# Performance work log

Measured on AMD Instinct MI355X. Metric: run time of the kernel, lower is better.

## Reference

```python
import jax, jax.numpy as jnp
from jax import lax
import numpy as np

B, L1, L2, H = 32, 128, 512, 256


def setup_inputs() -> dict:
    key = jax.random.key(0)
    ks = jax.random.split(key, 20)
    # valid lengths guarantee every row has at least one unmasked y position
    xlen = jax.random.randint(ks[0], (B,), L1 // 2, L1 + 1)
    ylen = jax.random.randint(ks[1], (B,), L2 // 2, L2 + 1)
    x_mask = (jnp.arange(L1)[None, :] >= xlen[:, None]).astype(jnp.int32)
    y_mask = (jnp.arange(L2)[None, :] >= ylen[:, None]).astype(jnp.int32)
    s = 0.05
    return {
        "x": jax.random.normal(ks[2], (B, L1, H), jnp.float32),
        "x_mask": x_mask,
        "y": jax.random.normal(ks[3], (B, L2, H), jnp.float32),
        "y_mask": y_mask,
        "h0": jax.random.uniform(ks[4], (B, H), jnp.float32),
        "c0": jax.random.uniform(ks[5], (B, H), jnp.float32),
        "Wq": jax.random.normal(ks[6], (H, H), jnp.float32) * s,
        "bq": jax.random.normal(ks[7], (H,), jnp.float32) * s,
        "Wup": jax.random.normal(ks[8], (H, H), jnp.float32) * s,
        "bup": jax.random.normal(ks[9], (H,), jnp.float32) * s,
        "Wvp": jax.random.normal(ks[10], (H, H), jnp.float32) * s,
        "bvp": jax.random.normal(ks[11], (H,), jnp.float32) * s,
        "Vw": jax.random.normal(ks[12], (1, H), jnp.float32) * s,
        "Vb": jax.random.normal(ks[13], (1,), jnp.float32) * s,
        "Wg": jax.random.normal(ks[14], (2 * H, 2 * H), jnp.float32) * s,
        "bg": jax.random.normal(ks[15], (2 * H,), jnp.float32) * s,
        "Wih": jax.random.normal(ks[16], (4 * H, 2 * H), jnp.float32) * s,
        "Whh": jax.random.normal(ks[17], (4 * H, H), jnp.float32) * s,
        "bih": jax.random.normal(ks[18], (4 * H,), jnp.float32) * s,
        "bhh": jax.random.normal(ks[19], (4 * H,), jnp.float32) * s,
    }


def _match_rnn(x, xm, y, ym, h0, c0, Wq, bq, Wup, bup, Wvp, bvp, Vw, Vb,
               Wg, bg, Wih, Whh, bih, bhh):
    # hoist time-invariant projections (original recomputes W_q(y) every step)
    y_proj = jnp.einsum("bld,hd->blh", y, Wq) + bq        # [B,L2,H]
    x_up = jnp.einsum("btd,hd->bth", x, Wup) + bup        # [B,L1,H]
    v = Vw[0]

    def step(carry, inp):
        h, c = carry
        x_t, xup_t, xm_t = inp                            # [B,H],[B,H],[B]
        hid = jnp.dot(h, Wvp.T) + bvp                     # [B,H]
        e = jnp.tanh(xup_t[:, None, :] + y_proj + hid[:, None, :])  # [B,L2,H]
        s = jnp.einsum("blh,h->bl", e, v) + Vb[0]         # [B,L2]
        s = jnp.where(ym, -jnp.inf, s)
        alpha = jax.nn.softmax(s, axis=-1)
        ct = jnp.einsum("bl,bld->bd", alpha, y)           # [B,H]
        merge = jnp.concatenate([x_t, ct], axis=-1)       # [B,2H]
        gt = jax.nn.sigmoid(jnp.dot(merge, Wg.T) + bg)
        li = jnp.where(xm_t[:, None], 0.0, gt * merge)
        # torch.nn.LSTMCell gate order: i, f, g, o
        gates = jnp.dot(li, Wih.T) + bih + jnp.dot(h, Whh.T) + bhh
        i, f, g, o = jnp.split(gates, 4, axis=-1)
        c_new = jax.nn.sigmoid(f) * c + jax.nn.sigmoid(i) * jnp.tanh(g)
        h_new = jax.nn.sigmoid(o) * jnp.tanh(c_new)
        h_new = jnp.where(xm_t[:, None], 0.0, h_new)
        return (h_new, c_new), h_new

    xs = (jnp.swapaxes(x, 0, 1), jnp.swapaxes(x_up, 0, 1),
          jnp.swapaxes(xm, 0, 1))
    _, hs = lax.scan(step, (h0, c0), xs)                  # hs: [L1,B,H]
    return jnp.swapaxes(hs, 0, 1)                         # [B,L1,H]


def reference(x, x_mask, y, y_mask, h0, c0, Wq, bq, Wup, bup, Wvp, bvp,
              Vw, Vb, Wg, bg, Wih, Whh, bih, bhh):
    xm = x_mask.astype(bool)
    ym = y_mask.astype(bool)
    return _match_rnn(x, xm, y, ym, h0, c0, Wq, bq, Wup, bup, Wvp, bvp,
                      Vw, Vb, Wg, bg, Wih, Whh, bih, bhh)
```

## Files before the change

### kernel.cpp

```cpp
#include <hip/hip_runtime.h>
#include <hip/hip_bf16.h>


#define B_ 32
#define L1_ 128
#define L2_ 512
#define H_ 256
#define GRP 8
#define TB 512
#define LOG2E_ 1.4426950408889634f

#define YP_OFF   0u
#define XUP_OFF  (8u << 20)
#define QP_OFF   (10u << 20)
#define CTP_OFF  (QP_OFF + (256u << 10))
#define ES_OFF   (CTP_OFF + (256u << 10))
#define LI_OFF   (ES_OFF + (4u << 10))
#define HB_OFF   (LI_OFF + (64u << 10))
#define BAR_OFF  (HB_OFF + (32u << 10))
#define WGB_OFF  (BAR_OFF + (4u << 10))
#define WIHB_OFF (WGB_OFF + (512u << 10))
#define WHHB_OFF (WIHB_OFF + (1024u << 10))

__device__ __forceinline__ float fexp2(float x) {
#if __has_builtin(__builtin_amdgcn_exp2f)
  return __builtin_amdgcn_exp2f(x);
#else
  return exp2f(x);
#endif
}
__device__ __forceinline__ float frcp(float x) {
#if __has_builtin(__builtin_amdgcn_rcpf)
  return __builtin_amdgcn_rcpf(x);
#else
  return 1.0f / x;
#endif
}
__device__ __forceinline__ float ftanh(float x) {
  return 1.0f - 2.0f * frcp(1.0f + fexp2(x * (2.0f * LOG2E_)));
}
__device__ __forceinline__ float fsig(float x) {
  return frcp(1.0f + fexp2(-x * LOG2E_));
}
__device__ __forceinline__ float dot4(float4 a, float4 b) {
  return a.x * b.x + a.y * b.y + a.z * b.z + a.w * b.w;
}
__device__ __forceinline__ float bfl(unsigned u) {
  return __uint_as_float(u << 16);
}
__device__ __forceinline__ float bfh(unsigned u) {
  return __uint_as_float(u & 0xffff0000u);
}
__device__ __forceinline__ unsigned short f2bf(float f) {
  __hip_bfloat16 b = __float2bfloat16(f);
  return *reinterpret_cast<unsigned short*>(&b);
}

__device__ __forceinline__ float cload(const float* p) {
  return __hip_atomic_load(p, __ATOMIC_RELAXED, __HIP_MEMORY_SCOPE_AGENT);
}
__device__ __forceinline__ void cstore(float* p, float v) {
  __hip_atomic_store(p, v, __ATOMIC_RELAXED, __HIP_MEMORY_SCOPE_AGENT);
}

__device__ __forceinline__ void group_barrier(unsigned* cnt, unsigned target) {
  asm volatile("s_waitcnt vmcnt(0)" ::: "memory");
  __syncthreads();
  if (threadIdx.x == 0) {
    __hip_atomic_fetch_add(cnt, 1u, __ATOMIC_RELAXED,
                           __HIP_MEMORY_SCOPE_AGENT);
    while (__hip_atomic_load(cnt, __ATOMIC_RELAXED,
                             __HIP_MEMORY_SCOPE_AGENT) < GRP * target) {
      __builtin_amdgcn_s_sleep(1);
    }
  }
  __syncthreads();
  asm volatile("" ::: "memory");
}

__global__ __launch_bounds__(256) void proj_kernel(
    const float* __restrict__ y, const float* __restrict__ Wq,
    const float* __restrict__ bq, const float* __restrict__ x,
    const float* __restrict__ Wup, const float* __restrict__ bup,
    __hip_bfloat16* __restrict__ yp, __hip_bfloat16* __restrict__ xup) {
  __shared__ float As[32 * 256];
  const int blk = blockIdx.x;
  const int tid = threadIdx.x;
  const float* src;
  const float* W;
  const float* bias;
  __hip_bfloat16* dst;
  int row0;
  if (blk < 512) {
    src = y; W = Wq; bias = bq; dst = yp; row0 = blk * 32;
  } else {
    src = x; W = Wup; bias = bup; dst = xup; row0 = (blk - 512) * 32;
  }
  const float4* s4 = (const float4*)(src + (size_t)row0 * H_);
  float4* A4 = (float4*)As;
#pragma unroll
  for (int i = 0; i < 8; ++i) A4[i * 256 + tid] = s4[i * 256 + tid];
  __syncthreads();

  const float4* w4 = (const float4*)(W + (size_t)tid * H_);
  float acc[32];
#pragma unroll
  for (int r = 0; r < 32; ++r) acc[r] = 0.0f;
  for (int kc = 0; kc < 64; ++kc) {
    float4 w = w4[kc];
#pragma unroll
    for (int r = 0; r < 32; ++r) acc[r] += dot4(A4[r * 64 + kc], w);
  }
  const float bb = bias[tid];
#pragma unroll 4
  for (int r = 0; r < 32; ++r)
    dst[(size_t)(row0 + r) * H_ + tid] = __float2bfloat16(acc[r] + bb);
}

__global__ __launch_bounds__(256) void wconv_kernel(
    const float* __restrict__ Wg, const float* __restrict__ Wih,
    const float* __restrict__ Whh, unsigned short* __restrict__ wgb,
    unsigned short* __restrict__ wihb, unsigned short* __restrict__ whhb) {
  const int e = blockIdx.x * 256 + threadIdx.x;
  const float* src;
  unsigned short* dst;
  int off;
  if (e < 65536) {
    src = Wg; dst = wgb; off = e;
  } else if (e < 196608) {
    src = Wih; dst = wihb; off = e - 65536;
  } else {
    src = Whh; dst = whhb; off = e - 196608;
  }
  float4 v = ((const float4*)src)[off];
  ushort4 o;
  o.x = f2bf(v.x); o.y = f2bf(v.y); o.z = f2bf(v.z); o.w = f2bf(v.w);
  ((ushort4*)dst)[off] = o;
}

__global__ __launch_bounds__(TB) void scan_kernel(
    const float* __restrict__ x, const int* __restrict__ x_mask,
    const float* __restrict__ y, const int* __restrict__ y_mask,
    const float* __restrict__ h0, const float* __restrict__ c0,
    const float* __restrict__ Wvp, const float* __restrict__ bvp,
    const float* __restrict__ Vw, const float* __restrict__ Vb,
    const float* __restrict__ bg, const float* __restrict__ bih,
    const float* __restrict__ bhh, char* __restrict__ ws,
    float* __restrict__ out) {
  const int blk = blockIdx.x;
  const int b = blk & 31;
  const int g = blk >> 5;
  const int tid = threadIdx.x;

  const __hip_bfloat16* yp = (const __hip_bfloat16*)(ws + YP_OFF);
  const unsigned short* xupb = (const unsigned short*)(ws + XUP_OFF);
  float* qp = (float*)(ws + QP_OFF);
  float* ctp = (float*)(ws + CTP_OFF);
  float* esb = (float*)(ws + ES_OFF);
  float* lib = (float*)(ws + LI_OFF);
  float* hb = (float*)(ws + HB_OFF);
  unsigned* cnt = (unsigned*)(ws + BAR_OFF) + b * 32;
  const unsigned short* wgb = (const unsigned short*)(ws + WGB_OFF);
  const unsigned short* wihb = (const unsigned short*)(ws + WIHB_OFF);
  const unsigned short* whhb = (const unsigned short*)(ws + WHHB_OFF);

  __shared__ uint4 yp_lds[64 * 32];
  __shared__ float y_lds[64 * 256];
  __shared__ __align__(16) float h_s[H_];
  __shared__ float q_s[H_];
  __shared__ float v_s[H_];
  __shared__ float bvp_s[H_];
  __shared__ float e_s[64];
  __shared__ __align__(16) float mg_s[2 * H_];
  __shared__ __align__(16) float li_s[2 * H_];
  __shared__ float gate_s[128];
  __shared__ float red_s[64 * 9];
  __shared__ float esum_s[8];
  __shared__ __align__(16) float c_s[32];
  __shared__ __align__(16) float hn_s[32];
  __shared__ float bg_s[64];
  __shared__ float bi_s[128];
  __shared__ int ym_s[64];
  __shared__ int xm_s[L1_];

  unsigned target = 0;

  {
    const uint4* src = (const uint4*)(yp + (size_t)(b * L2_ + g * 64) * H_);
    for (int k = tid; k < 64 * 32; k += TB) {
      int r = k >> 5, c = k & 31;
      yp_lds[r * 32 + (c ^ (r & 31))] = src[k];
    }
    const float4* ys = (const float4*)(y + (size_t)(b * L2_ + g * 64) * H_);
    float4* yd = (float4*)y_lds;
    for (int k = tid; k < 64 * 64; k += TB) yd[k] = ys[k];
  }
  if (tid < H_) {
    v_s[tid] = Vw[tid];
    bvp_s[tid] = bvp[tid];
  }
  if (tid < 64) {
    ym_s[tid] = y_mask[b * L2_ + g * 64 + tid];
    bg_s[tid] = bg[g * 64 + tid];
  }
  if (tid < 128) {
    xm_s[tid] = x_mask[b * L1_ + tid];
    const int grow = (tid >> 5) * H_ + g * 32 + (tid & 31);
    bi_s[tid] = bih[grow] + bhh[grow];
  }
  if (tid < 32) {
    float hv = h0[b * H_ + g * 32 + tid];
    c_s[tid] = c0[b * H_ + g * 32 + tid];
    hn_s[tid] = hv;
    cstore(&hb[b * H_ + g * 32 + tid], hv);
  }
  const float vb = Vb[0];
  __syncthreads();
  {
    const int j = tid >> 1, sub = tid & 1;
    const float4* w4 =
        (const float4*)(Wvp + (size_t)j * H_ + g * 32 + sub * 16);
    const float4* hv4 = (const float4*)(hn_s + sub * 16);
    float acc = 0.f;
#pragma unroll
    for (int i = 0; i < 4; ++i) acc += dot4(w4[i], hv4[i]);
    acc += __shfl_xor(acc, 1);
    if (sub == 0) cstore(&qp[(b * 8 + g) * H_ + j], acc);
  }
  group_barrier(cnt, ++target);

  for (int t = 0; t < L1_; ++t) {
    const int xm = xm_s[t];

    {
      const int j = tid & 255, half = tid >> 8;
      float acc = 0.f;
#pragma unroll
      for (int k = 0; k < 4; ++k)
        acc += cload(&qp[(b * 8 + half * 4 + k) * H_ + j]);
      red_s[half * 256 + j] = acc;
      if (tid < H_) h_s[tid] = cload(&hb[b * H_ + tid]);
    }
    __syncthreads();
    if (tid < H_) {
      q_s[tid] = red_s[tid] + red_s[256 + tid] + bvp_s[tid] +
                 bfl(xupb[(size_t)(b * L1_ + t) * H_ + tid]);
    }
    __syncthreads();

    {
      const int l = tid & 63, sub = tid >> 6;
      float acc = 0.f;
#pragma unroll
      for (int i = 0; i < 4; ++i) {
        uint4 u = yp_lds[l * 32 + ((sub * 4 + i) ^ (l & 31))];
        const int h = sub * 32 + i * 8;
        acc += v_s[h + 0] * ftanh(q_s[h + 0] + bfl(u.x));
        acc += v_s[h + 1] * ftanh(q_s[h + 1] + bfh(u.x));
        acc += v_s[h + 2] * ftanh(q_s[h + 2] + bfl(u.y));
        acc += v_s[h + 3] * ftanh(q_s[h + 3] + bfh(u.y));
        acc += v_s[h + 4] * ftanh(q_s[h + 4] + bfl(u.z));
        acc += v_s[h + 5] * ftanh(q_s[h + 5] + bfh(u.z));
        acc += v_s[h + 6] * ftanh(q_s[h + 6] + bfl(u.w));
        acc += v_s[h + 7] * ftanh(q_s[h + 7] + bfh(u.w));
      }
      red_s[l * 9 + sub] = acc;
    }
    __syncthreads();
    if (tid < 64) {
      float s = vb;
#pragma unroll
      for (int k = 0; k < 8; ++k) s += red_s[tid * 9 + k];
      float e = ym_s[tid] ? 0.f : fexp2(s * LOG2E_);
      e_s[tid] = e;
      float ss = e;
#pragma unroll
      for (int off = 32; off >= 1; off >>= 1) ss += __shfl_xor(ss, off);
      if (tid == 0) cstore(&esb[b * 8 + g], ss);
    }
    __syncthreads();

    {
      const int d = tid & 255, part = tid >> 8;
      float acc = 0.f;
#pragma unroll 8
      for (int i = 0; i < 32; ++i)
        acc += e_s[part * 32 + i] * y_lds[(part * 32 + i) * 256 + d];
      __syncthreads();
      red_s[tid] = acc;
    }
    __syncthreads();
    if (tid < H_)
      cstore(&ctp[(b * 8 + g) * H_ + tid], red_s[tid] + red_s[tid + 256]);
    group_barrier(cnt, ++target);

    if (tid < 8) esum_s[tid] = cload(&esb[b * 8 + tid]);
    {
      const int j = tid & 255, half = tid >> 8;
      float acc = 0.f;
#pragma unroll
      for (int k = 0; k < 4; ++k)
        acc += cload(&ctp[(b * 8 + half * 4 + k) * H_ + j]);
      red_s[half * 256 + j] = acc;
      if (tid < H_) mg_s[tid] = x[(size_t)(b * L1_ + t) * H_ + tid];
    }
    __syncthreads();
    if (tid < H_) {
      float tot = esum_s[0] + esum_s[1] + esum_s[2] + esum_s[3] + esum_s[4] +
                  esum_s[5] + esum_s[6] + esum_s[7];
      mg_s[H_ + tid] = (red_s[tid] + red_s[256 + tid]) * frcp(tot);
    }
    __syncthreads();

    {
      const int o = tid >> 3, sub = tid & 7;
      const uint4* wrow = (const uint4*)(wgb + (size_t)(g * 64 + o) * 512);
      const float4* m4 = (const float4*)mg_s;
      float acc = 0.f;
#pragma unroll
      for (int j = 0; j < 8; ++j) {
        uint4 u = wrow[sub + 8 * j];
        float4 ma = m4[(sub + 8 * j) * 2], mb = m4[(sub + 8 * j) * 2 + 1];
        acc += bfl(u.x) * ma.x + bfh(u.x) * ma.y + bfl(u.y) * ma.z +
               bfh(u.y) * ma.w + bfl(u.z) * mb.x + bfh(u.z) * mb.y +
               bfl(u.w) * mb.z + bfh(u.w) * mb.w;
      }
      acc += __shfl_xor(acc, 1);
      acc += __shfl_xor(acc, 2);
      acc += __shfl_xor(acc, 4);
      if (sub == 0) {
        float gt = fsig(acc + bg_s[o]);
        cstore(&lib[b * 512 + g * 64 + o], xm ? 0.f : gt * mg_s[g * 64 + o]);
      }
    }
    group_barrier(cnt, ++target);

    li_s[tid] = cload(&lib[b * 512 + tid]);
    __syncthreads();
    {
      const int r = tid >> 2, sub = tid & 3;
      const int grow = (r >> 5) * H_ + g * 32 + (r & 31);
      const uint4* wi = (const uint4*)(wihb + (size_t)grow * 512);
      const uint4* wh = (const uint4*)(whhb + (size_t)grow * 256);
      const float4* l4 = (const float4*)li_s;
      const float4* h4 = (const float4*)h_s;
      float acc = 0.f;
#pragma unroll
      for (int j = 0; j < 16; ++j) {
        uint4 u = wi[sub + 4 * j];
        float4 a = l4[(sub + 4 * j) * 2], c2 = l4[(sub + 4 * j) * 2 + 1];
        acc += bfl(u.x) * a.x + bfh(u.x) * a.y + bfl(u.y) * a.z +
               bfh(u.y) * a.w + bfl(u.z) * c2.x + bfh(u.z) * c2.y +
               bfl(u.w) * c2.z + bfh(u.w) * c2.w;
      }
#pragma unroll
      for (int j = 0; j < 8; ++j) {
        uint4 u = wh[sub + 4 * j];
        float4 a = h4[(sub + 4 * j) * 2], c2 = h4[(sub + 4 * j) * 2 + 1];
        acc += bfl(u.x) * a.x + bfh(u.x) * a.y + bfl(u.y) * a.z +
               bfh(u.y) * a.w + bfl(u.z) * c2.x + bfh(u.z) * c2.y +
               bfl(u.w) * c2.z + bfh(u.w) * c2.w;
      }
      acc += __shfl_xor(acc, 1);
      acc += __shfl_xor(acc, 2);
      if (sub == 0) gate_s[r] = acc + bi_s[r];
    }
    __syncthreads();
    if (tid < 32) {
      float ii = gate_s[tid], ff = gate_s[32 + tid];
      float gg = gate_s[64 + tid], oo = gate_s[96 + tid];
      float cn = fsig(ff) * c_s[tid] + fsig(ii) * ftanh(gg);
      float hn = xm ? 0.f : fsig(oo) * ftanh(cn);
      c_s[tid] = cn;
      hn_s[tid] = hn;
      cstore(&hb[b * H_ + g * 32 + tid], hn);
      out[(size_t)(b * L1_ + t) * H_ + g * 32 + tid] = hn;
    }
    __syncthreads();

    {
      const int j = tid >> 1, sub = tid & 1;
      const float4* w4 =
          (const float4*)(Wvp + (size_t)j * H_ + g * 32 + sub * 16);
      const float4* hv4 = (const float4*)(hn_s + sub * 16);
      float acc = 0.f;
#pragma unroll
      for (int i = 0; i < 4; ++i) acc += dot4(w4[i], hv4[i]);
      acc += __shfl_xor(acc, 1);
      if (sub == 0) cstore(&qp[(b * 8 + g) * H_ + j], acc);
    }
    group_barrier(cnt, ++target);
  }
}

extern "C" void kernel_launch(void* const* d_in, const int* in_sizes, int n_in,
                              void* d_out, int out_size, void* d_ws,
                              size_t ws_size, hipStream_t stream) {
  const float* x = (const float*)d_in[0];
  const int* x_mask = (const int*)d_in[1];
  const float* y = (const float*)d_in[2];
  const int* y_mask = (const int*)d_in[3];
  const float* h0 = (const float*)d_in[4];
  const float* c0 = (const float*)d_in[5];
  const float* Wq = (const float*)d_in[6];
  const float* bq = (const float*)d_in[7];
  const float* Wup = (const float*)d_in[8];
  const float* bup = (const float*)d_in[9];
  const float* Wvp = (const float*)d_in[10];
  const float* bvp = (const float*)d_in[11];
  const float* Vw = (const float*)d_in[12];
  const float* Vb = (const float*)d_in[13];
  const float* Wg = (const float*)d_in[14];
  const float* bg = (const float*)d_in[15];
  const float* Wih = (const float*)d_in[16];
  const float* Whh = (const float*)d_in[17];
  const float* bih = (const float*)d_in[18];
  const float* bhh = (const float*)d_in[19];

  float* out = (float*)d_out;
  char* ws = (char*)d_ws;

  hipMemsetAsync(ws + BAR_OFF, 0, 4096, stream);
  proj_kernel<<<dim3(640), dim3(256), 0, stream>>>(
      y, Wq, bq, x, Wup, bup, (__hip_bfloat16*)(ws + YP_OFF),
      (__hip_bfloat16*)(ws + XUP_OFF));
  wconv_kernel<<<dim3(1024), dim3(256), 0, stream>>>(
      Wg, Wih, Whh, (unsigned short*)(ws + WGB_OFF),
      (unsigned short*)(ws + WIHB_OFF), (unsigned short*)(ws + WHHB_OFF));
  scan_kernel<<<dim3(B_ * GRP), dim3(TB), 0, stream>>>(
      x, x_mask, y, y_mask, h0, c0, Wvp, bvp, Vw, Vb, bg, bih, bhh, ws, out);
}
```

Baseline: 1.539 ms.

## Cut per-step group barriers by replicating LSTM state and splitting gates by K

Each block in a batch group now keeps the full h and c state and recomputes the Wvp·h query projection locally from a bf16 copy of Wvp, so the per-step qp exchange and its group barrier go away. The LSTM gate matmul is split along the input dimension: each block computes partial sums for all 1024 gate rows from its own 64 li values and 32 h values, then writes them to global memory. After one barrier every block reduces the 8 partials and redundantly runs the cell update. This aims to halve inter-block barriers per timestep, in exchange for redundant Wvp work, more global partial-sum traffic and extra LDS use.

After: 2.424 ms. 1.57x slower.

```diff
diff --git a/kernel.cpp b/kernel.cpp
--- a/kernel.cpp
+++ b/kernel.cpp
@@ -12,15 +12,14 @@
 
 #define YP_OFF   0u
 #define XUP_OFF  (8u << 20)
-#define QP_OFF   (10u << 20)
-#define CTP_OFF  (QP_OFF + (256u << 10))
+#define CTP_OFF  (10u << 20)
 #define ES_OFF   (CTP_OFF + (256u << 10))
-#define LI_OFF   (ES_OFF + (4u << 10))
-#define HB_OFF   (LI_OFF + (64u << 10))
-#define BAR_OFF  (HB_OFF + (32u << 10))
+#define GPW_OFF  (ES_OFF + (4u << 10))
+#define BAR_OFF  (GPW_OFF + (1024u << 10))
 #define WGB_OFF  (BAR_OFF + (4u << 10))
 #define WIHB_OFF (WGB_OFF + (512u << 10))
 #define WHHB_OFF (WIHB_OFF + (1024u << 10))
+#define WVPB_OFF (WHHB_OFF + (512u << 10))
 
 __device__ __forceinline__ float fexp2(float x) {
 #if __has_builtin(__builtin_amdgcn_exp2f)
@@ -119,8 +118,9 @@
 
 __global__ __launch_bounds__(256) void wconv_kernel(
     const float* __restrict__ Wg, const float* __restrict__ Wih,
-    const float* __restrict__ Whh, unsigned short* __restrict__ wgb,
-    unsigned short* __restrict__ wihb, unsigned short* __restrict__ whhb) {
+    const float* __restrict__ Whh, const float* __restrict__ Wvp,
+    unsigned short* __restrict__ wgb, unsigned short* __restrict__ wihb,
+    unsigned short* __restrict__ whhb, unsigned short* __restrict__ wvpb) {
   const int e = blockIdx.x * 256 + threadIdx.x;
   const float* src;
   unsigned short* dst;
@@ -129,8 +129,10 @@
     src = Wg; dst = wgb; off = e;
   } else if (e < 196608) {
     src = Wih; dst = wihb; off = e - 65536;
+  } else if (e < 262144) {
+    src = Whh; dst = whhb; off = e - 196608;
   } else {
-    src = Whh; dst = whhb; off = e - 196608;
+    src = Wvp; dst = wvpb; off = e - 262144;
   }
   float4 v = ((const float4*)src)[off];
   ushort4 o;
@@ -142,11 +144,10 @@
     const float* __restrict__ x, const int* __restrict__ x_mask,
     const float* __restrict__ y, const int* __restrict__ y_mask,
     const float* __restrict__ h0, const float* __restrict__ c0,
-    const float* __restrict__ Wvp, const float* __restrict__ bvp,
-    const float* __restrict__ Vw, const float* __restrict__ Vb,
-    const float* __restrict__ bg, const float* __restrict__ bih,
-    const float* __restrict__ bhh, char* __restrict__ ws,
-    float* __restrict__ out) {
+    const float* __restrict__ bvp, const float* __restrict__ Vw,
+    const float* __restrict__ Vb, const float* __restrict__ bg,
+    const float* __restrict__ bih, const float* __restrict__ bhh,
+    char* __restrict__ ws, float* __restrict__ out) {
   const int blk = blockIdx.x;
   const int b = blk & 31;
   const int g = blk >> 5;
@@ -154,36 +155,32 @@
 
   const __hip_bfloat16* yp = (const __hip_bfloat16*)(ws + YP_OFF);
   const unsigned short* xupb = (const unsigned short*)(ws + XUP_OFF);
-  float* qp = (float*)(ws + QP_OFF);
   float* ctp = (float*)(ws + CTP_OFF);
   float* esb = (float*)(ws + ES_OFF);
-  float* lib = (float*)(ws + LI_OFF);
-  float* hb = (float*)(ws + HB_OFF);
+  float* gpw = (float*)(ws + GPW_OFF);
   unsigned* cnt = (unsigned*)(ws + BAR_OFF) + b * 32;
   const unsigned short* wgb = (const unsigned short*)(ws + WGB_OFF);
   const unsigned short* wihb = (const unsigned short*)(ws + WIHB_OFF);
   const unsigned short* whhb = (const unsigned short*)(ws + WHHB_OFF);
+  const unsigned short* wvpb = (const unsigned short*)(ws + WVPB_OFF);
 
   __shared__ uint4 yp_lds[64 * 32];
   __shared__ float y_lds[64 * 256];
   __shared__ __align__(16) float h_s[H_];
+  __shared__ __align__(16) float c_s[H_];
   __shared__ float q_s[H_];
   __shared__ float v_s[H_];
   __shared__ float bvp_s[H_];
+  __shared__ __align__(16) float mg_s[2 * H_];
+  __shared__ __align__(16) float li_s[64];
+  __shared__ float gate_s[1024];
+  __shared__ float bi_s[1024];
+  __shared__ float red_s[64 * 9];
   __shared__ float e_s[64];
-  __shared__ __align__(16) float mg_s[2 * H_];
-  __shared__ __align__(16) float li_s[2 * H_];
-  __shared__ float gate_s[128];
-  __shared__ float red_s[64 * 9];
   __shared__ float esum_s[8];
-  __shared__ __align__(16) float c_s[32];
-  __shared__ __align__(16) float hn_s[32];
   __shared__ float bg_s[64];
-  __shared__ float bi_s[128];
   __shared__ int ym_s[64];
   __shared__ int xm_s[L1_];
-
-  unsigned target = 0;
 
   {
     const uint4* src = (const uint4*)(yp + (size_t)(b * L2_ + g * 64) * H_);
@@ -198,53 +195,40 @@
   if (tid < H_) {
     v_s[tid] = Vw[tid];
     bvp_s[tid] = bvp[tid];
+    h_s[tid] = h0[b * H_ + tid];
+    c_s[tid] = c0[b * H_ + tid];
   }
   if (tid < 64) {
     ym_s[tid] = y_mask[b * L2_ + g * 64 + tid];
     bg_s[tid] = bg[g * 64 + tid];
   }
-  if (tid < 128) {
-    xm_s[tid] = x_mask[b * L1_ + tid];
-    const int grow = (tid >> 5) * H_ + g * 32 + (tid & 31);
-    bi_s[tid] = bih[grow] + bhh[grow];
-  }
-  if (tid < 32) {
-    float hv = h0[b * H_ + g * 32 + tid];
-    c_s[tid] = c0[b * H_ + g * 32 + tid];
-    hn_s[tid] = hv;
-    cstore(&hb[b * H_ + g * 32 + tid], hv);
-  }
+  if (tid < 128) xm_s[tid] = x_mask[b * L1_ + tid];
+  bi_s[tid] = bih[tid] + bhh[tid];
+  bi_s[tid + 512] = bih[tid + 512] + bhh[tid + 512];
   const float vb = Vb[0];
   __syncthreads();
-  {
-    const int j = tid >> 1, sub = tid & 1;
-    const float4* w4 =
-        (const float4*)(Wvp + (size_t)j * H_ + g * 32 + sub * 16);
-    const float4* hv4 = (const float4*)(hn_s + sub * 16);
-    float acc = 0.f;
-#pragma unroll
-    for (int i = 0; i < 4; ++i) acc += dot4(w4[i], hv4[i]);
-    acc += __shfl_xor(acc, 1);
-    if (sub == 0) cstore(&qp[(b * 8 + g) * H_ + j], acc);
-  }
-  group_barrier(cnt, ++target);
+
+  unsigned target = 0;
 
   for (int t = 0; t < L1_; ++t) {
     const int xm = xm_s[t];
 
     {
-      const int j = tid & 255, half = tid >> 8;
+      const int j = tid >> 1, sub = tid & 1;
+      const uint4* wv = (const uint4*)(wvpb + (size_t)j * H_) + sub * 16;
+      const float4* h4 = (const float4*)h_s + sub * 32;
       float acc = 0.f;
 #pragma unroll
-      for (int k = 0; k < 4; ++k)
-        acc += cload(&qp[(b * 8 + half * 4 + k) * H_ + j]);
-      red_s[half * 256 + j] = acc;
-      if (tid < H_) h_s[tid] = cload(&hb[b * H_ + tid]);
-    }
-    __syncthreads();
-    if (tid < H_) {
-      q_s[tid] = red_s[tid] + red_s[256 + tid] + bvp_s[tid] +
-                 bfl(xupb[(size_t)(b * L1_ + t) * H_ + tid]);
+      for (int k = 0; k < 16; ++k) {
+        uint4 u = wv[k];
+        float4 a = h4[2 * k], c2 = h4[2 * k + 1];
+        acc += bfl(u.x) * a.x + bfh(u.x) * a.y + bfl(u.y) * a.z +
+               bfh(u.y) * a.w + bfl(u.z) * c2.x + bfh(u.z) * c2.y +
+               bfl(u.w) * c2.z + bfh(u.w) * c2.w;
+      }
+      acc += __shfl_xor(acc, 1);
+      if (sub == 0)
+        q_s[j] = acc + bvp_s[j] + bfl(xupb[(size_t)(b * L1_ + t) * H_ + j]);
     }
     __syncthreads();
 
@@ -286,7 +270,6 @@
 #pragma unroll 8
       for (int i = 0; i < 32; ++i)
         acc += e_s[part * 32 + i] * y_lds[(part * 32 + i) * 256 + d];
-      __syncthreads();
       red_s[tid] = acc;
     }
     __syncthreads();
@@ -330,66 +313,62 @@
       acc += __shfl_xor(acc, 4);
       if (sub == 0) {
         float gt = fsig(acc + bg_s[o]);
-        cstore(&lib[b * 512 + g * 64 + o], xm ? 0.f : gt * mg_s[g * 64 + o]);
+        li_s[o] = xm ? 0.f : gt * mg_s[g * 64 + o];
       }
     }
+    __syncthreads();
+
+    {
+      const float4* l4 = (const float4*)li_s;
+      const float4* hb4 = (const float4*)(h_s + g * 32);
+#pragma unroll
+      for (int rr = 0; rr < 2; ++rr) {
+        const int r = tid + rr * 512;
+        const uint4* wi = (const uint4*)wihb + (size_t)r * 64 + g * 8;
+        const uint4* wh = (const uint4*)whhb + (size_t)r * 32 + g * 4;
+        float acc = 0.f;
+#pragma unroll
+        for (int j = 0; j < 8; ++j) {
+          uint4 u = wi[j];
+          float4 a = l4[2 * j], c2 = l4[2 * j + 1];
+          acc += bfl(u.x) * a.x + bfh(u.x) * a.y + bfl(u.y) * a.z +
+                 bfh(u.y) * a.w + bfl(u.z) * c2.x + bfh(u.z) * c2.y +
+                 bfl(u.w) * c2.z + bfh(u.w) * c2.w;
+        }
+#pragma unroll
+        for (int j = 0; j < 4; ++j) {
+          uint4 u = wh[j];
+          float4 a = hb4[2 * j], c2 = hb4[2 * j + 1];
+          acc += bfl(u.x) * a.x + bfh(u.x) * a.y + bfl(u.y) * a.z +
+                 bfh(u.y) * a.w + bfl(u.z) * c2.x + bfh(u.z) * c2.y +
+                 bfl(u.w) * c2.z + bfh(u.w) * c2.w;
+        }
+        cstore(&gpw[(size_t)(b * 8 + g) * 1024 + r], acc);
+      }
+    }
     group_barrier(cnt, ++target);
 
-    li_s[tid] = cload(&lib[b * 512 + tid]);
-    __syncthreads();
-    {
-      const int r = tid >> 2, sub = tid & 3;
-      const int grow = (r >> 5) * H_ + g * 32 + (r & 31);
-      const uint4* wi = (const uint4*)(wihb + (size_t)grow * 512);
-      const uint4* wh = (const uint4*)(whhb + (size_t)grow * 256);
-      const float4* l4 = (const float4*)li_s;
-      const float4* h4 = (const float4*)h_s;
-      float acc = 0.f;
-#pragma unroll
-      for (int j = 0; j < 16; ++j) {
-        uint4 u = wi[sub + 4 * j];
-        float4 a = l4[(sub + 4 * j) * 2], c2 = l4[(sub + 4 * j) * 2 + 1];
-        acc += bfl(u.x) * a.x + bfh(u.x) * a.y + bfl(u.y) * a.z +
-               bfh(u.y) * a.w + bfl(u.z) * c2.x + bfh(u.z) * c2.y +
-               bfl(u.w) * c2.z + bfh(u.w) * c2.w;
-      }
-#pragma unroll
-      for (int j = 0; j < 8; ++j) {
-        uint4 u = wh[sub + 4 * j];
-        float4 a = h4[(sub + 4 * j) * 2], c2 = h4[(sub + 4 * j) * 2 + 1];
-        acc += bfl(u.x) * a.x + bfh(u.x) * a.y + bfl(u.y) * a.z +
-               bfh(u.y) * a.w + bfl(u.z) * c2.x + bfh(u.z) * c2.y +
-               bfl(u.w) * c2.z + bfh(u.w) * c2.w;
-      }
-      acc += __shfl_xor(acc, 1);
-      acc += __shfl_xor(acc, 2);
-      if (sub == 0) gate_s[r] = acc + bi_s[r];
-    }
-    __syncthreads();
-    if (tid < 32) {
-      float ii = gate_s[tid], ff = gate_s[32 + tid];
-      float gg = gate_s[64 + tid], oo = gate_s[96 + tid];
+#pragma unroll
+    for (int rr = 0; rr < 2; ++rr) {
+      const int r = tid + rr * 512;
+      float s = bi_s[r];
+#pragma unroll
+      for (int g2 = 0; g2 < 8; ++g2)
+        s += cload(&gpw[(size_t)(b * 8 + g2) * 1024 + r]);
+      gate_s[r] = s;
+    }
+    __syncthreads();
+    if (tid < H_) {
+      float ii = gate_s[tid], ff = gate_s[H_ + tid];
+      float gg = gate_s[2 * H_ + tid], oo = gate_s[3 * H_ + tid];
       float cn = fsig(ff) * c_s[tid] + fsig(ii) * ftanh(gg);
       float hn = xm ? 0.f : fsig(oo) * ftanh(cn);
       c_s[tid] = cn;
-      hn_s[tid] = hn;
-      cstore(&hb[b * H_ + g * 32 + tid], hn);
-      out[(size_t)(b * L1_ + t) * H_ + g * 32 + tid] = hn;
-    }
-    __syncthreads();
-
-    {
-      const int j = tid >> 1, sub = tid & 1;
-      const float4* w4 =
-          (const float4*)(Wvp + (size_t)j * H_ + g * 32 + sub * 16);
-      const float4* hv4 = (const float4*)(hn_s + sub * 16);
-      float acc = 0.f;
-#pragma unroll
-      for (int i = 0; i < 4; ++i) acc += dot4(w4[i], hv4[i]);
-      acc += __shfl_xor(acc, 1);
-      if (sub == 0) cstore(&qp[(b * 8 + g) * H_ + j], acc);
-    }
-    group_barrier(cnt, ++target);
+      h_s[tid] = hn;
+      if ((tid >> 5) == g)
+        out[(size_t)(b * L1_ + t) * H_ + tid] = hn;
+    }
+    __syncthreads();
   }
 }
 
@@ -424,9 +403,10 @@
   proj_kernel<<<dim3(640), dim3(256), 0, stream>>>(
       y, Wq, bq, x, Wup, bup, (__hip_bfloat16*)(ws + YP_OFF),
       (__hip_bfloat16*)(ws + XUP_OFF));
-  wconv_kernel<<<dim3(1024), dim3(256), 0, stream>>>(
-      Wg, Wih, Whh, (unsigned short*)(ws + WGB_OFF),
-      (unsigned short*)(ws + WIHB_OFF), (unsigned short*)(ws + WHHB_OFF));
+  wconv_kernel<<<dim3(1088), dim3(256), 0, stream>>>(
+      Wg, Wih, Whh, Wvp, (unsigned short*)(ws + WGB_OFF),
+      (unsigned short*)(ws + WIHB_OFF), (unsigned short*)(ws + WHHB_OFF),
+      (unsigned short*)(ws + WVPB_OFF));
   scan_kernel<<<dim3(B_ * GRP), dim3(TB), 0, stream>>>(
-      x, x_mask, y, y_mask, h0, c0, Wvp, bvp, Vw, Vb, bg, bih, bhh, ws, out);
-}
+      x, x_mask, y, y_mask, h0, c0, bvp, Vw, Vb, bg, bih, bhh, ws, out);
+}
```
